# Kernel optimization log

Hardware: AMD Instinct MI355X
Metric: run time of the kernel (lower is better)

Reference implementation:

```python
import jax, jax.numpy as jnp
import numpy as np
import math

B, T, C, H = 8, 1024, 768, 12
HD = C // H  # 64


def setup_inputs() -> dict:
    key = jax.random.key(0)
    k1, k2, k3 = jax.random.split(key, 3)
    x = jax.random.normal(k1, (B, T, C), dtype=jnp.float32)
    W_attn = jax.random.normal(k2, (C, 3 * C), dtype=jnp.float32) * 0.02
    b_attn = jnp.zeros((3 * C,), dtype=jnp.float32)
    W_proj = jax.random.normal(k3, (C, C), dtype=jnp.float32) * (0.02 / math.sqrt(2 * 12))
    b_proj = jnp.zeros((C,), dtype=jnp.float32)
    return {"x": x, "W_attn": W_attn, "b_attn": b_attn, "W_proj": W_proj, "b_proj": b_proj}


def reference(x, W_attn, b_attn, W_proj, b_proj):
    Bx, Tx, Cx = x.shape
    qkv = x @ W_attn + b_attn                        # [B,T,3C]
    # faithful to original: reshape to (B,T,H,3*HD) then split last axis
    qkv = qkv.reshape(Bx, Tx, H, 3 * HD).transpose(0, 2, 1, 3)  # [B,H,T,3*HD]
    q, k, v = jnp.split(qkv, 3, axis=-1)             # each [B,H,T,HD]
    att = jnp.einsum('bhqd,bhkd->bhqk', q, k) / math.sqrt(HD)
    causal = jnp.tril(jnp.ones((Tx, Tx), dtype=bool))
    att = jnp.where(causal, att, -jnp.inf)
    att = jax.nn.softmax(att, axis=-1)
    y = jnp.einsum('bhqk,bhkd->bhqd', att, v)        # [B,H,T,HD]
    y = y.transpose(0, 2, 1, 3).reshape(Bx, Tx, Cx)  # [B,T,C]
    return y @ W_proj + b_proj
```

## Files before the change

kernel.cpp:

```cpp
#include <hip/hip_runtime.h>
#include <hip/hip_bf16.h>


#define TDIM 1024
#define CDIM 768
#define NDIM 2304

typedef __attribute__((ext_vector_type(8))) short bf16x8;
typedef __attribute__((ext_vector_type(8))) unsigned short u16x8;
typedef __attribute__((ext_vector_type(4))) float f32x4;

__device__ __forceinline__ unsigned short f2bf(float f) {
    unsigned int u;
    __builtin_memcpy(&u, &f, 4);
    u += 0x7FFFu + ((u >> 16) & 1u);
    return (unsigned short)(u >> 16);
}

__device__ __forceinline__ void async_copy16(void* lds, const void* g) {
    __builtin_amdgcn_global_load_lds(
        (const __attribute__((address_space(1))) void*)g,
        (__attribute__((address_space(3))) void*)lds, 16, 0, 0);
}

__global__ __launch_bounds__(256) void cast_x(const float* __restrict__ x,
                                              unsigned short* __restrict__ xb) {
    const size_t i = ((size_t)blockIdx.x * 256 + threadIdx.x) * 4;
    float4 v = *(const float4*)&x[i];
    ushort4 s;
    s.x = f2bf(v.x); s.y = f2bf(v.y); s.z = f2bf(v.z); s.w = f2bf(v.w);
    *(ushort4*)&xb[i] = s;
}

template <int N>
__global__ __launch_bounds__(256) void transpose_cast(const float* __restrict__ W,
                                                      unsigned short* __restrict__ Wt) {
    __shared__ float tile[32][33];
    const int n0 = blockIdx.x * 32;
    const int k0 = blockIdx.y * 32;
    const int tx = threadIdx.x & 31;
    const int ty = threadIdx.x >> 5;
#pragma unroll
    for (int i = 0; i < 4; ++i)
        tile[ty + i * 8][tx] = W[(size_t)(k0 + ty + i * 8) * N + n0 + tx];
    __syncthreads();
#pragma unroll
    for (int i = 0; i < 4; ++i)
        Wt[(size_t)(n0 + ty + i * 8) * CDIM + k0 + tx] = f2bf(tile[tx][ty + i * 8]);
}

__global__ __launch_bounds__(256) void qkv_mfma(
    const unsigned short* __restrict__ xb, const unsigned short* __restrict__ Wt,
    const float* __restrict__ bias,
    unsigned short* __restrict__ Q, unsigned short* __restrict__ Kd,
    unsigned short* __restrict__ Vt)
{
    const int n0 = blockIdx.x * 128;
    const int m0 = blockIdx.y * 128;
    const int tid = threadIdx.x;
    const int lane = tid & 63;
    const int w = tid >> 6;
    const int wm = w & 1;
    const int wn = w >> 1;
    const int lm = lane & 15;
    const int lq = lane >> 4;

    __shared__ __align__(16) unsigned short As[128 * 32];
    __shared__ __align__(16) unsigned short Bs[128 * 32];
    __shared__ __align__(16) unsigned short Es[4][16][72];

    f32x4 acc[4][4] = {};

    const int srow = lane >> 2;
    const int schunk = lane & 3;

    for (int k0 = 0; k0 < CDIM; k0 += 32) {
        __syncthreads();
#pragma unroll
        for (int c = 0; c < 2; ++c) {
            const int rbase = c * 64 + w * 16;
            async_copy16(&As[rbase * 32],
                         &xb[(size_t)(m0 + rbase + srow) * CDIM + k0 + schunk * 8]);
            async_copy16(&Bs[rbase * 32],
                         &Wt[(size_t)(n0 + rbase + srow) * CDIM + k0 + schunk * 8]);
        }
        __syncthreads();

        bf16x8 a[4], b[4];
#pragma unroll
        for (int mi = 0; mi < 4; ++mi)
            a[mi] = *(const bf16x8*)&As[(wm * 64 + mi * 16 + lm) * 32 + lq * 8];
#pragma unroll
        for (int ni = 0; ni < 4; ++ni)
            b[ni] = *(const bf16x8*)&Bs[(wn * 64 + ni * 16 + lm) * 32 + lq * 8];
#pragma unroll
        for (int mi = 0; mi < 4; ++mi)
#pragma unroll
            for (int ni = 0; ni < 4; ++ni)
                acc[mi][ni] = __builtin_amdgcn_mfma_f32_16x16x32_bf16(
                    a[mi], b[ni], acc[mi][ni], 0, 0, 0);
    }

    const int ga = (n0 >> 6) + wn;
    const int which = ga % 3;
    const int h = (n0 + wn * 64) / 192;
    float bb[4];
#pragma unroll
    for (int ni = 0; ni < 4; ++ni)
        bb[ni] = bias[n0 + wn * 64 + ni * 16 + lm];

    if (which == 2) {
#pragma unroll
        for (int ni = 0; ni < 4; ++ni) {
            const int d = ni * 16 + lm;
#pragma unroll
            for (int mi = 0; mi < 4; ++mi) {
                const int gm0 = m0 + wm * 64 + mi * 16 + lq * 4;
                const int bidx = gm0 >> 10;
                const int t0 = gm0 & 1023;
                ushort4 sv;
                sv.x = f2bf(acc[mi][ni][0] + bb[ni]);
                sv.y = f2bf(acc[mi][ni][1] + bb[ni]);
                sv.z = f2bf(acc[mi][ni][2] + bb[ni]);
                sv.w = f2bf(acc[mi][ni][3] + bb[ni]);
                *(ushort4*)&Vt[(((size_t)bidx * 12 + h) * 64 + d) * TDIM + t0] = sv;
            }
        }
    } else {
        unsigned short* dst = (which == 0) ? Q : Kd;
        const int erow = lane >> 2;
        const int ecol = lane & 3;
#pragma unroll
        for (int mi = 0; mi < 4; ++mi) {
#pragma unroll
            for (int r = 0; r < 4; ++r)
#pragma unroll
                for (int ni = 0; ni < 4; ++ni)
                    Es[w][lq * 4 + r][ni * 16 + lm] = f2bf(acc[mi][ni][r] + bb[ni]);
            const int t = m0 + wm * 64 + mi * 16 + erow;
            const int bidx = t >> 10;
            const int tt = t & 1023;
            unsigned short* drow = &dst[(((size_t)bidx * 12 + h) * TDIM + tt) * 64];
            u16x8 v0 = *(const u16x8*)&Es[w][erow][ecol * 16];
            u16x8 v1 = *(const u16x8*)&Es[w][erow][ecol * 16 + 8];
            *(u16x8*)&drow[ecol * 16] = v0;
            *(u16x8*)&drow[ecol * 16 + 8] = v1;
        }
    }
}

#define ATTN_TILE(aq, q0t, qt_t, l_p, o) do {                                   \
    const bool diag_ = (kt == (qt_t));                                          \
    float pf[4][4];                                                             \
    _Pragma("unroll")                                                           \
    for (int nt = 0; nt < 4; ++nt) {                                            \
        f32x4 s = {};                                                           \
        _Pragma("unroll")                                                       \
        for (int kc = 0; kc < 2; ++kc) {                                        \
            bf16x8 bfrag = *(const bf16x8*)&Ks[nt * 16 + lm][kc * 32 + lq * 8]; \
            s = __builtin_amdgcn_mfma_f32_16x16x32_bf16(aq[kc], bfrag, s, 0, 0, 0); \
        }                                                                       \
        const int keyg = kbase + nt * 16 + lm;                                  \
        _Pragma("unroll")                                                       \
        for (int r = 0; r < 4; ++r) {                                           \
            float p = __builtin_amdgcn_exp2f(s[r] * SC);                        \
            if (diag_) {                                                        \
                const int qg = (q0t) + w * 16 + lq * 4 + r;                     \
                if (keyg > qg) p = 0.f;                                         \
            }                                                                   \
            pf[nt][r] = p;                                                      \
        }                                                                       \
    }                                                                           \
    _Pragma("unroll")                                                           \
    for (int r = 0; r < 4; ++r) {                                               \
        l_p[r] += pf[0][r] + pf[1][r] + pf[2][r] + pf[3][r];                    \
        _Pragma("unroll")                                                       \
        for (int nt = 0; nt < 4; ++nt)                                          \
            Ps[w][lq * 4 + r][nt * 16 + lm] = f2bf(pf[nt][r]);                  \
    }                                                                           \
    {                                                                           \
        bf16x8 ap[2];                                                           \
        _Pragma("unroll")                                                       \
        for (int kc = 0; kc < 2; ++kc)                                          \
            ap[kc] = *(const bf16x8*)&Ps[w][lm][kc * 32 + lq * 8];              \
        _Pragma("unroll")                                                       \
        for (int nt = 0; nt < 4; ++nt) {                                        \
            _Pragma("unroll")                                                   \
            for (int kc = 0; kc < 2; ++kc) {                                    \
                bf16x8 bv = *(const bf16x8*)&Vts[nt * 16 + lm][kc * 32 + lq * 8]; \
                o[nt] = __builtin_amdgcn_mfma_f32_16x16x32_bf16(ap[kc], bv, o[nt], 0, 0, 0); \
            }                                                                   \
        }                                                                       \
    }                                                                           \
} while (0)

#define ATTN_EPI(q0t, l_p, o) do {                                              \
    _Pragma("unroll")                                                           \
    for (int r = 0; r < 4; ++r) {                                               \
        float l = l_p[r];                                                       \
        _Pragma("unroll")                                                       \
        for (int off = 1; off < 16; off <<= 1) l += __shfl_xor(l, off);         \
        const float inv = 1.0f / l;                                             \
        const int qg = (q0t) + w * 16 + lq * 4 + r;                             \
        _Pragma("unroll")                                                       \
        for (int nt = 0; nt < 4; ++nt)                                          \
            Yb[(size_t)qg * 64 + nt * 16 + lm] = f2bf(o[nt][r] * inv);          \
    }                                                                           \
} while (0)

__global__ __launch_bounds__(256) void attn_mfma(
    const unsigned short* __restrict__ Q, const unsigned short* __restrict__ K,
    const unsigned short* __restrict__ Vt, unsigned short* __restrict__ Y)
{
    const int pi = blockIdx.x;
    const int bh = blockIdx.y;
    const int qtA = pi, qtB = 15 - pi;
    const int q0A = qtA * 64, q0B = qtB * 64;
    const int tid = threadIdx.x;
    const int lane = tid & 63;
    const int w = tid >> 6;
    const int lm = lane & 15;
    const int lq = lane >> 4;

    __shared__ __align__(16) unsigned short Ks[64][72];
    __shared__ __align__(16) unsigned short Vts[64][72];
    __shared__ __align__(16) unsigned short Ps[4][16][72];

    const unsigned short* Qb = Q + (size_t)bh * TDIM * 64;
    const unsigned short* Kb = K + (size_t)bh * TDIM * 64;
    const unsigned short* Vtb = Vt + (size_t)bh * 64 * TDIM;
    unsigned short* Yb = Y + (size_t)bh * TDIM * 64;

    bf16x8 aqA[2], aqB[2];
#pragma unroll
    for (int kc = 0; kc < 2; ++kc) {
        aqA[kc] = *(const bf16x8*)&Qb[(size_t)(q0A + w * 16 + lm) * 64 + kc * 32 + lq * 8];
        aqB[kc] = *(const bf16x8*)&Qb[(size_t)(q0B + w * 16 + lm) * 64 + kc * 32 + lq * 8];
    }

    float lA[4] = {}, lB[4] = {};
    f32x4 oA[4] = {}, oB[4] = {};

    const float SC = 0.125f * 1.44269504f;
    const int nktA = qtA + 1;
    const int nktB = qtB + 1;

    for (int kt = 0; kt < nktB; ++kt) {
        const int kbase = kt * 64;
        __syncthreads();
#pragma unroll
        for (int it = 0; it < 2; ++it) {
            const int idx = tid + it * 256;
            const int r = idx >> 3;
            const int c = idx & 7;
            *(u16x8*)&Ks[r][c * 8] =
                *(const u16x8*)&Kb[(size_t)(kbase + r) * 64 + c * 8];
            *(u16x8*)&Vts[r][c * 8] =
                *(const u16x8*)&Vtb[(size_t)r * TDIM + kbase + c * 8];
        }
        __syncthreads();

        ATTN_TILE(aqB, q0B, qtB, lB, oB);
        if (kt < nktA) ATTN_TILE(aqA, q0A, qtA, lA, oA);
    }

    ATTN_EPI(q0A, lA, oA);
    ATTN_EPI(q0B, lB, oB);
}

__global__ __launch_bounds__(256) void proj_mfma(
    const unsigned short* __restrict__ Y, const unsigned short* __restrict__ Wt,
    const float* __restrict__ bias, float* __restrict__ out)
{
    const int n0 = blockIdx.x * 128;
    const int m0 = blockIdx.y * 128;
    const int tid = threadIdx.x;
    const int lane = tid & 63;
    const int w = tid >> 6;
    const int wm = w & 1;
    const int wn = w >> 1;
    const int lm = lane & 15;
    const int lq = lane >> 4;

    __shared__ __align__(16) unsigned short As[128 * 32];
    __shared__ __align__(16) unsigned short Bs[128 * 32];

    f32x4 acc[4][4] = {};

    const int srow = lane >> 2;
    const int schunk = lane & 3;

    for (int k0 = 0; k0 < CDIM; k0 += 32) {
        const int h = k0 >> 6;
        const int inner = k0 & 63;
        __syncthreads();
#pragma unroll
        for (int c = 0; c < 2; ++c) {
            const int rbase = c * 64 + w * 16;
            const int m = m0 + rbase + srow;
            const int bidx = m >> 10;
            const int t = m & 1023;
            async_copy16(&As[rbase * 32],
                         &Y[(((size_t)bidx * 12 + h) * TDIM + t) * 64 + inner + schunk * 8]);
            async_copy16(&Bs[rbase * 32],
                         &Wt[(size_t)(n0 + rbase + srow) * CDIM + k0 + schunk * 8]);
        }
        __syncthreads();

        bf16x8 a[4], b[4];
#pragma unroll
        for (int mi = 0; mi < 4; ++mi)
            a[mi] = *(const bf16x8*)&As[(wm * 64 + mi * 16 + lm) * 32 + lq * 8];
#pragma unroll
        for (int ni = 0; ni < 4; ++ni)
            b[ni] = *(const bf16x8*)&Bs[(wn * 64 + ni * 16 + lm) * 32 + lq * 8];
#pragma unroll
        for (int mi = 0; mi < 4; ++mi)
#pragma unroll
            for (int ni = 0; ni < 4; ++ni)
                acc[mi][ni] = __builtin_amdgcn_mfma_f32_16x16x32_bf16(
                    a[mi], b[ni], acc[mi][ni], 0, 0, 0);
    }

#pragma unroll
    for (int ni = 0; ni < 4; ++ni) {
        const int gn = n0 + wn * 64 + ni * 16 + lm;
        const float bb = bias[gn];
#pragma unroll
        for (int mi = 0; mi < 4; ++mi) {
#pragma unroll
            for (int r = 0; r < 4; ++r) {
                const int gm = m0 + wm * 64 + mi * 16 + lq * 4 + r;
                out[(size_t)gm * CDIM + gn] = acc[mi][ni][r] + bb;
            }
        }
    }
}

extern "C" void kernel_launch(void* const* d_in, const int* in_sizes, int n_in,
                              void* d_out, int out_size, void* d_ws, size_t ws_size,
                              hipStream_t stream) {
    const float* x      = (const float*)d_in[0];
    const float* W_attn = (const float*)d_in[1];
    const float* b_attn = (const float*)d_in[2];
    const float* W_proj = (const float*)d_in[3];
    const float* b_proj = (const float*)d_in[4];
    float* out = (float*)d_out;

    const size_t per = (size_t)8 * 12 * 1024 * 64;
    unsigned short* Q   = (unsigned short*)d_ws;
    unsigned short* K   = Q + per;
    unsigned short* Vt  = K + per;
    unsigned short* xb  = Vt + per;
    unsigned short* Wta = xb + (size_t)8192 * CDIM;
    unsigned short* Wtp = Wta + (size_t)NDIM * CDIM;

    cast_x<<<dim3(6144), 256, 0, stream>>>(x, xb);
    transpose_cast<NDIM><<<dim3(72, 24), 256, 0, stream>>>(W_attn, Wta);
    transpose_cast<CDIM><<<dim3(24, 24), 256, 0, stream>>>(W_proj, Wtp);

    qkv_mfma<<<dim3(18, 64), 256, 0, stream>>>(xb, Wta, b_attn, Q, K, Vt);
    attn_mfma<<<dim3(8, 96), 256, 0, stream>>>(Q, K, Vt, Q);
    proj_mfma<<<dim3(6, 64), 256, 0, stream>>>(Q, Wtp, b_proj, out);
}
```

Baseline: 203.9 us.

## Rewrite QKV GEMM as 256x256 double-buffered, XOR-swizzled, barrier-interleaved pipeline

The QKV projection GEMM moves from 128x128 tiles with 256 threads and a load-sync-compute loop to 256x256 tiles with 512 threads (8 waves). It uses a double-buffered 128KB LDS with XOR-swizzled layout and K-steps of 64. Async global-to-LDS copies are interleaved with MFMA quadrants under fine-grained barriers, vmcnt waits and s_setprio. Blocks are remapped for L2 locality. This aims to hide load latency and raise arithmetic intensity, at the cost of high register and LDS pressure, which limits occupancy, and fewer blocks (288) than CUs times two.

```diff
diff --git a/kernel.cpp b/kernel.cpp
--- a/kernel.cpp
+++ b/kernel.cpp
@@ -49,73 +49,174 @@
         Wt[(size_t)(n0 + ty + i * 8) * CDIM + k0 + tx] = f2bf(tile[tx][ty + i * 8]);
 }
 
-__global__ __launch_bounds__(256) void qkv_mfma(
+__global__ __launch_bounds__(512, 2) void qkv_mfma(
     const unsigned short* __restrict__ xb, const unsigned short* __restrict__ Wt,
     const float* __restrict__ bias,
     unsigned short* __restrict__ Q, unsigned short* __restrict__ Kd,
     unsigned short* __restrict__ Vt)
 {
-    const int n0 = blockIdx.x * 128;
-    const int m0 = blockIdx.y * 128;
+    const int wg = ((int)blockIdx.x & 7) * 36 + ((int)blockIdx.x >> 3);
+    const int bx = wg % 9;
+    const int by = wg / 9;
+    const int n0 = bx * 256;
+    const int m0 = by * 256;
     const int tid = threadIdx.x;
     const int lane = tid & 63;
     const int w = tid >> 6;
-    const int wm = w & 1;
-    const int wn = w >> 1;
+    const int wm = w >> 2;
+    const int wn = w & 3;
     const int lm = lane & 15;
     const int lq = lane >> 4;
 
-    __shared__ __align__(16) unsigned short As[128 * 32];
-    __shared__ __align__(16) unsigned short Bs[128 * 32];
-    __shared__ __align__(16) unsigned short Es[4][16][72];
-
-    f32x4 acc[4][4] = {};
-
-    const int srow = lane >> 2;
-    const int schunk = lane & 3;
-
-    for (int k0 = 0; k0 < CDIM; k0 += 32) {
-        __syncthreads();
-#pragma unroll
-        for (int c = 0; c < 2; ++c) {
-            const int rbase = c * 64 + w * 16;
-            async_copy16(&As[rbase * 32],
-                         &xb[(size_t)(m0 + rbase + srow) * CDIM + k0 + schunk * 8]);
-            async_copy16(&Bs[rbase * 32],
-                         &Wt[(size_t)(n0 + rbase + srow) * CDIM + k0 + schunk * 8]);
-        }
-        __syncthreads();
-
-        bf16x8 a[4], b[4];
-#pragma unroll
-        for (int mi = 0; mi < 4; ++mi)
-            a[mi] = *(const bf16x8*)&As[(wm * 64 + mi * 16 + lm) * 32 + lq * 8];
-#pragma unroll
-        for (int ni = 0; ni < 4; ++ni)
-            b[ni] = *(const bf16x8*)&Bs[(wn * 64 + ni * 16 + lm) * 32 + lq * 8];
-#pragma unroll
-        for (int mi = 0; mi < 4; ++mi)
-#pragma unroll
-            for (int ni = 0; ni < 4; ++ni)
-                acc[mi][ni] = __builtin_amdgcn_mfma_f32_16x16x32_bf16(
-                    a[mi], b[ni], acc[mi][ni], 0, 0, 0);
-    }
-
-    const int ga = (n0 >> 6) + wn;
+    __shared__ __align__(16) unsigned short lds[65536];
+
+    float bb[4];
+#pragma unroll
+    for (int ni = 0; ni < 4; ++ni) bb[ni] = bias[n0 + wn * 64 + ni * 16 + lm];
+
+    f32x4 acc[8][4] = {};
+    bf16x8 aF[4][2], bF0[2][2], bF1[2][2];
+
+    const int eo = lq ^ (lm & 7);
+    const unsigned short* pA[2][2];
+    const unsigned short* pB[2][2];
+#pragma unroll
+    for (int p = 0; p < 2; ++p)
+#pragma unroll
+        for (int ks = 0; ks < 2; ++ks) {
+            pA[p][ks] = &lds[p * 32768 + (wm * 128 + lm) * 64 + (eo ^ (4 * ks)) * 8];
+            pB[p][ks] = &lds[p * 32768 + 16384 + (wn * 64 + lm) * 64 + (eo ^ (4 * ks)) * 8];
+        }
+
+#define LDA(pp, mh)                                                             \
+    _Pragma("unroll")                                                           \
+    for (int mi2 = 0; mi2 < 4; ++mi2)                                           \
+        _Pragma("unroll")                                                       \
+        for (int ks = 0; ks < 2; ++ks)                                          \
+            aF[mi2][ks] = *(const bf16x8*)(pA[pp][ks] + ((mh) * 64 + mi2 * 16) * 64)
+
+#define LDB(pp, nh, BF)                                                         \
+    _Pragma("unroll")                                                           \
+    for (int nj = 0; nj < 2; ++nj)                                              \
+        _Pragma("unroll")                                                       \
+        for (int ks = 0; ks < 2; ++ks)                                          \
+            BF[nj][ks] = *(const bf16x8*)(pB[pp][ks] + ((nh) * 32 + nj * 16) * 64)
+
+#define MM(mh, nh, BF)                                                          \
+    _Pragma("unroll")                                                           \
+    for (int mi2 = 0; mi2 < 4; ++mi2)                                           \
+        _Pragma("unroll")                                                       \
+        for (int nj = 0; nj < 2; ++nj)                                          \
+            _Pragma("unroll")                                                   \
+            for (int ks = 0; ks < 2; ++ks)                                      \
+                acc[(mh) * 4 + mi2][(nh) * 2 + nj] =                            \
+                    __builtin_amdgcn_mfma_f32_16x16x32_bf16(                    \
+                        aF[mi2][ks], BF[nj][ks],                                \
+                        acc[(mh) * 4 + mi2][(nh) * 2 + nj], 0, 0, 0)
+
+#define STG_A(pp, kt, mh)                                                       \
+    do {                                                                        \
+        _Pragma("unroll")                                                       \
+        for (int j = 0; j < 2; ++j) {                                           \
+            const int nbase = w * 128 + j * 64;                                 \
+            const int nl = nbase + lane;                                        \
+            const int rl = nl >> 3;                                             \
+            const int cc = (nl & 7) ^ (rl & 7);                                 \
+            const int rowG = (rl & 63) + (mh) * 64 + ((rl >> 6) << 7);          \
+            async_copy16(&lds[(pp) * 32768 +                                    \
+                              ((mh) * 512 + (nbase & 511) +                     \
+                               ((nbase >= 512) ? 1024 : 0)) * 8],               \
+                         &xb[(size_t)(m0 + rowG) * CDIM + (kt) * 64 + cc * 8]); \
+        }                                                                       \
+    } while (0)
+
+#define STG_B(pp, kt, nh)                                                       \
+    do {                                                                        \
+        _Pragma("unroll")                                                       \
+        for (int j = 0; j < 2; ++j) {                                           \
+            const int nbase = w * 128 + j * 64;                                 \
+            const int nl = nbase + lane;                                        \
+            const int rl = nl >> 3;                                             \
+            const int cc = (nl & 7) ^ (rl & 7);                                 \
+            const int rowG = ((rl >> 5) << 6) + (nh) * 32 + (rl & 31);          \
+            async_copy16(&lds[(pp) * 32768 + 16384 +                            \
+                              (((nbase >> 8) << 9) + (nh) * 256 +               \
+                               (nbase & 255)) * 8],                             \
+                         &Wt[(size_t)(n0 + rowG) * CDIM + (kt) * 64 + cc * 8]); \
+        }                                                                       \
+    } while (0)
+
+#define BAR_MID()                                                               \
+    __builtin_amdgcn_s_barrier();                                               \
+    asm volatile("s_waitcnt lgkmcnt(0)" ::: "memory");                          \
+    __builtin_amdgcn_s_setprio(1)
+
+#define BAR_END()                                                               \
+    __builtin_amdgcn_s_setprio(0);                                              \
+    __builtin_amdgcn_s_barrier()
+
+#define BAR_END_VM()                                                            \
+    __builtin_amdgcn_s_setprio(0);                                              \
+    asm volatile("s_waitcnt vmcnt(6)" ::: "memory");                            \
+    __builtin_amdgcn_s_barrier()
+
+    STG_A(0, 0, 0); STG_B(0, 0, 0); STG_B(0, 0, 1); STG_A(0, 0, 1);
+    STG_A(1, 1, 0); STG_B(1, 1, 0); STG_B(1, 1, 1);
+    asm volatile("s_waitcnt vmcnt(6)" ::: "memory");
+    __builtin_amdgcn_s_barrier();
+
+#pragma unroll 1
+    for (int it = 0; it < 6; ++it) {
+        const int t1 = 2 * it + 1;
+        const int s2 = (2 * it + 2 < 12) ? (2 * it + 2) : 11;
+        const int s3 = (2 * it + 3 < 12) ? (2 * it + 3) : 11;
+        LDA(0, 0); LDB(0, 0, bF0);
+        STG_A(1, t1, 1);
+        BAR_MID(); MM(0, 0, bF0); BAR_END();
+        LDB(0, 1, bF1);
+        STG_A(0, s2, 0);
+        BAR_MID(); MM(0, 1, bF1); BAR_END();
+        LDA(0, 1);
+        STG_B(0, s2, 0);
+        BAR_MID(); MM(1, 1, bF1); BAR_END();
+        STG_B(0, s2, 1);
+        BAR_MID(); MM(1, 0, bF0); BAR_END_VM();
+        LDA(1, 0); LDB(1, 0, bF0);
+        STG_A(0, s2, 1);
+        BAR_MID(); MM(0, 0, bF0); BAR_END();
+        LDB(1, 1, bF1);
+        STG_A(1, s3, 0);
+        BAR_MID(); MM(0, 1, bF1); BAR_END();
+        LDA(1, 1);
+        STG_B(1, s3, 0);
+        BAR_MID(); MM(1, 1, bF1); BAR_END();
+        STG_B(1, s3, 1);
+        BAR_MID(); MM(1, 0, bF0); BAR_END_VM();
+    }
+
+#undef LDA
+#undef LDB
+#undef MM
+#undef STG_A
+#undef STG_B
+#undef BAR_MID
+#undef BAR_END
+#undef BAR_END_VM
+
+    asm volatile("s_waitcnt vmcnt(0)" ::: "memory");
+    __builtin_amdgcn_s_barrier();
+
+    const int ga = bx * 4 + wn;
     const int which = ga % 3;
-    const int h = (n0 + wn * 64) / 192;
-    float bb[4];
-#pragma unroll
-    for (int ni = 0; ni < 4; ++ni)
-        bb[ni] = bias[n0 + wn * 64 + ni * 16 + lm];
+    const int h = ga / 3;
 
     if (which == 2) {
 #pragma unroll
         for (int ni = 0; ni < 4; ++ni) {
             const int d = ni * 16 + lm;
 #pragma unroll
-            for (int mi = 0; mi < 4; ++mi) {
-                const int gm0 = m0 + wm * 64 + mi * 16 + lq * 4;
+            for (int mi = 0; mi < 8; ++mi) {
+                const int gm0 = m0 + wm * 128 + mi * 16 + lq * 4;
                 const int bidx = gm0 >> 10;
                 const int t0 = gm0 & 1023;
                 ushort4 sv;
@@ -128,21 +229,22 @@
         }
     } else {
         unsigned short* dst = (which == 0) ? Q : Kd;
+        unsigned short* Es = &lds[w * 1152];
         const int erow = lane >> 2;
         const int ecol = lane & 3;
 #pragma unroll
-        for (int mi = 0; mi < 4; ++mi) {
+        for (int mi = 0; mi < 8; ++mi) {
 #pragma unroll
             for (int r = 0; r < 4; ++r)
 #pragma unroll
                 for (int ni = 0; ni < 4; ++ni)
-                    Es[w][lq * 4 + r][ni * 16 + lm] = f2bf(acc[mi][ni][r] + bb[ni]);
-            const int t = m0 + wm * 64 + mi * 16 + erow;
+                    Es[(lq * 4 + r) * 72 + ni * 16 + lm] = f2bf(acc[mi][ni][r] + bb[ni]);
+            const int t = m0 + wm * 128 + mi * 16 + erow;
             const int bidx = t >> 10;
             const int tt = t & 1023;
             unsigned short* drow = &dst[(((size_t)bidx * 12 + h) * TDIM + tt) * 64];
-            u16x8 v0 = *(const u16x8*)&Es[w][erow][ecol * 16];
-            u16x8 v1 = *(const u16x8*)&Es[w][erow][ecol * 16 + 8];
+            u16x8 v0 = *(const u16x8*)&Es[erow * 72 + ecol * 16];
+            u16x8 v1 = *(const u16x8*)&Es[erow * 72 + ecol * 16 + 8];
             *(u16x8*)&drow[ecol * 16] = v0;
             *(u16x8*)&drow[ecol * 16 + 8] = v1;
         }
@@ -359,7 +461,7 @@
     transpose_cast<NDIM><<<dim3(72, 24), 256, 0, stream>>>(W_attn, Wta);
     transpose_cast<CDIM><<<dim3(24, 24), 256, 0, stream>>>(W_proj, Wtp);
 
-    qkv_mfma<<<dim3(18, 64), 256, 0, stream>>>(xb, Wta, b_attn, Q, K, Vt);
+    qkv_mfma<<<dim3(288), 512, 0, stream>>>(xb, Wta, b_attn, Q, K, Vt);
     attn_mfma<<<dim3(8, 96), 256, 0, stream>>>(Q, K, Vt, Q);
     proj_mfma<<<dim3(6, 64), 256, 0, stream>>>(Q, Wtp, b_proj, out);
 }
```

Measured after the change: 195.7 us. -4.0%, faster.

## Triple-buffer QKV GEMM with async LDS loads, 128x256 tiles, swizzle and XCD remap

Applied to the files above, without the earlier changes.

Restructures the QKV projection GEMM to use 512-thread blocks with 128x256 output tiles and a 3-stage LDS ring buffer. Global-to-LDS async copies for future k-steps are issued before computing the current one, using vmcnt waits and one barrier per tile. It also XOR-swizzles LDS chunks to reduce bank conflicts, remaps block IDs across XCDs, and raises MFMA priority. Larger LDS use (72KB) limits occupancy, and the clamped tail iterations redundantly reload the last tile.

```diff
diff --git a/kernel.cpp b/kernel.cpp
--- a/kernel.cpp
+++ b/kernel.cpp
@@ -49,65 +49,111 @@
         Wt[(size_t)(n0 + ty + i * 8) * CDIM + k0 + tx] = f2bf(tile[tx][ty + i * 8]);
 }
 
-__global__ __launch_bounds__(256) void qkv_mfma(
+__global__ __launch_bounds__(512, 4) void qkv_mfma(
     const unsigned short* __restrict__ xb, const unsigned short* __restrict__ Wt,
     const float* __restrict__ bias,
     unsigned short* __restrict__ Q, unsigned short* __restrict__ Kd,
     unsigned short* __restrict__ Vt)
 {
-    const int n0 = blockIdx.x * 128;
-    const int m0 = blockIdx.y * 128;
+    const int wg = ((int)blockIdx.x & 7) * 72 + ((int)blockIdx.x >> 3);
+    const int bx = wg % 9;
+    const int by = wg / 9;
+    const int n0 = bx * 256;
+    const int m0 = by * 128;
     const int tid = threadIdx.x;
     const int lane = tid & 63;
     const int w = tid >> 6;
-    const int wm = w & 1;
-    const int wn = w >> 1;
+    const int wm = w >> 2;
+    const int wn = w & 3;
     const int lm = lane & 15;
     const int lq = lane >> 4;
 
-    __shared__ __align__(16) unsigned short As[128 * 32];
-    __shared__ __align__(16) unsigned short Bs[128 * 32];
-    __shared__ __align__(16) unsigned short Es[4][16][72];
+    __shared__ __align__(16) unsigned short lds[36864];
+
+    float bb[4];
+#pragma unroll
+    for (int ni = 0; ni < 4; ++ni) bb[ni] = bias[n0 + wn * 64 + ni * 16 + lm];
 
     f32x4 acc[4][4] = {};
 
-    const int srow = lane >> 2;
-    const int schunk = lane & 3;
-
-    for (int k0 = 0; k0 < CDIM; k0 += 32) {
-        __syncthreads();
-#pragma unroll
-        for (int c = 0; c < 2; ++c) {
-            const int rbase = c * 64 + w * 16;
-            async_copy16(&As[rbase * 32],
-                         &xb[(size_t)(m0 + rbase + srow) * CDIM + k0 + schunk * 8]);
-            async_copy16(&Bs[rbase * 32],
-                         &Wt[(size_t)(n0 + rbase + srow) * CDIM + k0 + schunk * 8]);
-        }
-        __syncthreads();
-
-        bf16x8 a[4], b[4];
-#pragma unroll
-        for (int mi = 0; mi < 4; ++mi)
-            a[mi] = *(const bf16x8*)&As[(wm * 64 + mi * 16 + lm) * 32 + lq * 8];
-#pragma unroll
-        for (int ni = 0; ni < 4; ++ni)
-            b[ni] = *(const bf16x8*)&Bs[(wn * 64 + ni * 16 + lm) * 32 + lq * 8];
-#pragma unroll
-        for (int mi = 0; mi < 4; ++mi)
-#pragma unroll
-            for (int ni = 0; ni < 4; ++ni)
-                acc[mi][ni] = __builtin_amdgcn_mfma_f32_16x16x32_bf16(
-                    a[mi], b[ni], acc[mi][ni], 0, 0, 0);
-    }
-
-    const int ga = (n0 >> 6) + wn;
+    const int eo = lq ^ ((lm >> 1) & 3);
+    int aoffc[4], boffc[4];
+#pragma unroll
+    for (int mi = 0; mi < 4; ++mi)
+        aoffc[mi] = (wm * 64 + mi * 16 + lm) * 32 + eo * 8;
+#pragma unroll
+    for (int ni = 0; ni < 4; ++ni)
+        boffc[ni] = 4096 + (wn * 64 + ni * 16 + lm) * 32 + eo * 8;
+
+    const int rowA = tid >> 2;
+    const int ccA = (tid & 3) ^ ((rowA >> 1) & 3);
+    const int srcA = rowA * CDIM + ccA * 8;
+    int srcB[2];
+#pragma unroll
+    for (int j = 0; j < 2; ++j) {
+        const int lin = j * 512 + tid;
+        const int rowB = lin >> 2;
+        const int ccB = (lin & 3) ^ ((rowB >> 1) & 3);
+        srcB[j] = rowB * CDIM + ccB * 8;
+    }
+    const unsigned short* xbb = xb + (size_t)m0 * CDIM;
+    const unsigned short* Wtb = Wt + (size_t)n0 * CDIM;
+
+#define STAGE(p, kt)                                                            \
+    do {                                                                        \
+        async_copy16(&lds[(p) * 12288 + w * 512], &xbb[srcA + (kt) * 32]);      \
+        _Pragma("unroll")                                                       \
+        for (int j = 0; j < 2; ++j)                                             \
+            async_copy16(&lds[(p) * 12288 + 4096 + j * 4096 + w * 512],         \
+                         &Wtb[srcB[j] + (kt) * 32]);                            \
+    } while (0)
+
+#define TILE(p, ktn)                                                            \
+    do {                                                                        \
+        STAGE((p + 2) % 3, ktn);                                                \
+        bf16x8 a[4], b[4];                                                      \
+        _Pragma("unroll")                                                       \
+        for (int mi = 0; mi < 4; ++mi)                                          \
+            a[mi] = *(const bf16x8*)&lds[(p) * 12288 + aoffc[mi]];              \
+        _Pragma("unroll")                                                       \
+        for (int ni = 0; ni < 4; ++ni)                                          \
+            b[ni] = *(const bf16x8*)&lds[(p) * 12288 + boffc[ni]];              \
+        __builtin_amdgcn_s_setprio(1);                                          \
+        _Pragma("unroll")                                                       \
+        for (int mi = 0; mi < 4; ++mi)                                          \
+            _Pragma("unroll")                                                   \
+            for (int ni = 0; ni < 4; ++ni)                                      \
+                acc[mi][ni] = __builtin_amdgcn_mfma_f32_16x16x32_bf16(          \
+                    a[mi], b[ni], acc[mi][ni], 0, 0, 0);                        \
+        __builtin_amdgcn_s_setprio(0);                                          \
+        asm volatile("s_waitcnt vmcnt(3)" ::: "memory");                        \
+        __builtin_amdgcn_s_barrier();                                           \
+    } while (0)
+
+    STAGE(0, 0);
+    STAGE(1, 1);
+    asm volatile("s_waitcnt vmcnt(3)" ::: "memory");
+    __builtin_amdgcn_s_barrier();
+
+#pragma unroll 1
+    for (int it = 0; it < 8; ++it) {
+        const int k2 = (3 * it + 2 < 24) ? 3 * it + 2 : 23;
+        const int k3 = (3 * it + 3 < 24) ? 3 * it + 3 : 23;
+        const int k4 = (3 * it + 4 < 24) ? 3 * it + 4 : 23;
+        TILE(0, k2);
+        TILE(1, k3);
+        TILE(2, k4);
+    }
+
+#undef STAGE
+#undef TILE
+
+    asm volatile("s_waitcnt vmcnt(0)" ::: "memory");
+    __builtin_amdgcn_s_barrier();
+
+    const int ga = bx * 4 + wn;
     const int which = ga % 3;
-    const int h = (n0 + wn * 64) / 192;
-    float bb[4];
-#pragma unroll
-    for (int ni = 0; ni < 4; ++ni)
-        bb[ni] = bias[n0 + wn * 64 + ni * 16 + lm];
+    const int h = ga / 3;
 
     if (which == 2) {
 #pragma unroll
@@ -128,6 +174,7 @@
         }
     } else {
         unsigned short* dst = (which == 0) ? Q : Kd;
+        unsigned short* Es = &lds[w * 1152];
         const int erow = lane >> 2;
         const int ecol = lane & 3;
 #pragma unroll
@@ -136,13 +183,13 @@
             for (int r = 0; r < 4; ++r)
 #pragma unroll
                 for (int ni = 0; ni < 4; ++ni)
-                    Es[w][lq * 4 + r][ni * 16 + lm] = f2bf(acc[mi][ni][r] + bb[ni]);
+                    Es[(lq * 4 + r) * 72 + ni * 16 + lm] = f2bf(acc[mi][ni][r] + bb[ni]);
             const int t = m0 + wm * 64 + mi * 16 + erow;
             const int bidx = t >> 10;
             const int tt = t & 1023;
             unsigned short* drow = &dst[(((size_t)bidx * 12 + h) * TDIM + tt) * 64];
-            u16x8 v0 = *(const u16x8*)&Es[w][erow][ecol * 16];
-            u16x8 v1 = *(const u16x8*)&Es[w][erow][ecol * 16 + 8];
+            u16x8 v0 = *(const u16x8*)&Es[erow * 72 + ecol * 16];
+            u16x8 v1 = *(const u16x8*)&Es[erow * 72 + ecol * 16 + 8];
             *(u16x8*)&drow[ecol * 16] = v0;
             *(u16x8*)&drow[ecol * 16 + 8] = v1;
         }
@@ -359,7 +406,7 @@
     transpose_cast<NDIM><<<dim3(72, 24), 256, 0, stream>>>(W_attn, Wta);
     transpose_cast<CDIM><<<dim3(24, 24), 256, 0, stream>>>(W_proj, Wtp);
 
-    qkv_mfma<<<dim3(18, 64), 256, 0, stream>>>(xb, Wta, b_attn, Q, K, Vt);
+    qkv_mfma<<<dim3(576), 512, 0, stream>>>(xb, Wta, b_attn, Q, K, Vt);
     attn_mfma<<<dim3(8, 96), 256, 0, stream>>>(Q, K, Vt, Q);
     proj_mfma<<<dim3(6, 64), 256, 0, stream>>>(Q, Wtp, b_proj, out);
 }
```

After: 187.4 us. 8.1% less time.
